# Performance work log

Hardware: AMD Instinct MI355X
Metric: run time of the kernel (lower is better)

## Reference

```python
import jax, jax.numpy as jnp
import numpy as np

H = 2048          # hidden_size
NH = 32           # num_attention_heads
NKV = 8           # num_key_value_heads
HD = H // NH      # head_dim = 64
GROUPS = NH // NKV
B, S = 1, 4096


def setup_inputs() -> dict:
    key = jax.random.key(0)
    k1, k2, k3, k4, k5 = jax.random.split(key, 5)
    hidden_states = jax.random.normal(k1, (B, S, H), dtype=jnp.float32)
    # additive causal mask [B, 1, S, S]
    causal = jnp.tril(jnp.ones((S, S), dtype=bool))
    attention_mask = jnp.where(causal, 0.0, jnp.finfo(jnp.float32).min)[None, None].astype(jnp.float32)
    scale = 0.02
    Wq = jax.random.normal(k2, (H, H), dtype=jnp.float32) * scale
    Wk = jax.random.normal(k3, (NKV * HD, H), dtype=jnp.float32) * scale
    Wv = jax.random.normal(k4, (NKV * HD, H), dtype=jnp.float32) * scale
    Wo = jax.random.normal(k5, (H, H), dtype=jnp.float32) * scale
    return {"hidden_states": hidden_states, "attention_mask": attention_mask,
            "Wq": Wq, "Wk": Wk, "Wv": Wv, "Wo": Wo}


def reference(hidden_states, attention_mask, Wq, Wk, Wv, Wo):
    bsz, q_len, _ = hidden_states.shape
    # projections (nn.Linear: x @ W.T)
    q = (hidden_states @ Wq.T).reshape(bsz, q_len, NH, HD).transpose(0, 2, 1, 3)   # [B,NH,S,HD]
    k = (hidden_states @ Wk.T).reshape(bsz, q_len, NKV, HD).transpose(0, 2, 1, 3)  # [B,NKV,S,HD]
    v = (hidden_states @ Wv.T).reshape(bsz, q_len, NKV, HD).transpose(0, 2, 1, 3)
    # repeat_kv: expand each KV head GROUPS times
    k = jnp.repeat(k, GROUPS, axis=1)  # [B,NH,S,HD]
    v = jnp.repeat(v, GROUPS, axis=1)
    attn_weights = jnp.einsum('bhqd,bhkd->bhqk', q, k) / jnp.sqrt(jnp.float32(HD))
    attn_weights = attn_weights + attention_mask
    attn_weights = jax.nn.softmax(attn_weights.astype(jnp.float32), axis=-1).astype(q.dtype)
    attn_output = jnp.einsum('bhqk,bhkd->bhqd', attn_weights, v)
    attn_output = attn_output.transpose(0, 2, 1, 3).reshape(bsz, q_len, H)
    return attn_output @ Wo.T
```

## Files before the change

kernel.cpp:

```cpp
#include <hip/hip_runtime.h>
#include <stdint.h>

#define S_LEN  4096
#define HDIM   2048
#define NHEADS 32
#define NKVH   8
#define HDSZ   64
#define KVDIM  (NKVH * HDSZ)
#define QKN    (HDIM + KVDIM)

typedef __bf16 v8bf16 __attribute__((ext_vector_type(8)));
typedef short  v4s    __attribute__((ext_vector_type(4)));
typedef float  v4f32  __attribute__((ext_vector_type(4)));

__device__ __forceinline__ unsigned short f2bf(float f) {
    uint32_t u = __builtin_bit_cast(uint32_t, f);
    uint32_t r = (u + 0x7fffu + ((u >> 16) & 1u)) >> 16;
    return (unsigned short)r;
}

__device__ __forceinline__ uint32_t pack_bf16(float a, float b) {
#if __has_builtin(__builtin_amdgcn_cvt_pk_bf16_f32)
    auto r = __builtin_amdgcn_cvt_pk_bf16_f32(a, b);
    return __builtin_bit_cast(uint32_t, r);
#else
    uint32_t ua = __builtin_bit_cast(uint32_t, a) + 0x8000u;
    uint32_t ub = __builtin_bit_cast(uint32_t, b) + 0x8000u;
    return (ua >> 16) | (ub & 0xffff0000u);
#endif
}

__device__ __forceinline__ float fast_exp2(float x) {
#if __has_builtin(__builtin_amdgcn_exp2f)
    return __builtin_amdgcn_exp2f(x);
#else
    float r; asm("v_exp_f32 %0, %1" : "=v"(r) : "v"(x)); return r;
#endif
}

__device__ __forceinline__ void async_load16(const void* g, void* l) {
    __builtin_amdgcn_global_load_lds((const __attribute__((address_space(1))) void*)g,
                                     (__attribute__((address_space(3))) void*)l,
                                     16, 0, 0);
}

#define SEG0 2097152
#define SEG1 3145728
#define SEG2 3407872
#define SEG3 3670016
#define SEGT 4718592
__global__ void cvt_all(const float* __restrict__ x,  const float* __restrict__ wq,
                        const float* __restrict__ wk, const float* __restrict__ wv,
                        const float* __restrict__ wo,
                        ushort4* __restrict__ xb, ushort4* __restrict__ wqkb,
                        ushort4* __restrict__ wvb, ushort4* __restrict__ wob,
                        float qscale)
{
    int i = blockIdx.x * blockDim.x + threadIdx.x;
    if (i >= SEGT) return;
    const float4* src; ushort4* dst; float s = 1.0f; int loc;
    if (i < SEG0)      { src = (const float4*)x;  dst = xb;   loc = i; }
    else if (i < SEG1) { src = (const float4*)wq; dst = wqkb; loc = i - SEG0; s = qscale; }
    else if (i < SEG2) { src = (const float4*)wk; dst = wqkb + 1048576; loc = i - SEG1; }
    else if (i < SEG3) { src = (const float4*)wv; dst = wvb;  loc = i - SEG2; }
    else               { src = (const float4*)wo; dst = wob;  loc = i - SEG3; }
    float4 f = src[loc];
    uint2 o;
    o.x = pack_bf16(f.x * s, f.y * s);
    o.y = pack_bf16(f.z * s, f.w * s);
    dst[loc] = __builtin_bit_cast(ushort4, o);
}


#define STAGE_A(buf, kh, t)                                                       \
    do {                                                                          \
        async_load16(A + aBase + (size_t)(t) * 64 + (kh) * 32,                    \
                     &smem[(buf) * 16384 + (kh) * 8192 + ldsSt]);                 \
        async_load16(A + aBase + (size_t)128 * Kd + (size_t)(t) * 64 + (kh) * 32, \
                     &smem[(buf) * 16384 + (kh) * 8192 + ldsSt + 4096]);          \
    } while (0)
#define STAGE_B(buf, kh, t)                                                       \
    do {                                                                          \
        async_load16(Bp + bBase + (size_t)(t) * 64 + (kh) * 32,                   \
                     &smem[32768 + (buf) * 16384 + (kh) * 8192 + ldsSt]);         \
        async_load16(Bp + bBase + (size_t)128 * Kd + (size_t)(t) * 64 + (kh) * 32,\
                     &smem[32768 + (buf) * 16384 + (kh) * 8192 + ldsSt + 4096]);  \
    } while (0)

#define LOAD_AF(khoff)                                                            \
    do {                                                                          \
        _Pragma("unroll")                                                         \
        for (int mi = 0; mi < 8; ++mi)                                            \
            af[mi] = *(const v8bf16*)&smem[curA + (khoff) + aRd + mi * 512];      \
    } while (0)

#define MFMA_PAIR(khoff, NI)                                                      \
    do {                                                                          \
        v8bf16 _b0 = *(const v8bf16*)&smem[curB + (khoff) + bRd + (NI) * 512];    \
        v8bf16 _b1 = *(const v8bf16*)&smem[curB + (khoff) + bRd + (NI) * 512 + 512];\
        __builtin_amdgcn_s_setprio(1);                                            \
        _Pragma("unroll")                                                         \
        for (int mi = 0; mi < 8; ++mi) {                                          \
            acc[mi][(NI)]     = __builtin_amdgcn_mfma_f32_16x16x32_bf16(af[mi], _b0, acc[mi][(NI)], 0, 0, 0);     \
            acc[mi][(NI) + 1] = __builtin_amdgcn_mfma_f32_16x16x32_bf16(af[mi], _b1, acc[mi][(NI) + 1], 0, 0, 0); \
        }                                                                         \
        __builtin_amdgcn_s_setprio(0);                                            \
    } while (0)

#define FENCE_BAR()                                                               \
    do {                                                                          \
        __builtin_amdgcn_sched_barrier(0);                                        \
        __builtin_amdgcn_s_barrier();                                             \
        __builtin_amdgcn_sched_barrier(0);                                        \
    } while (0)

#define WAITV(N) asm volatile("s_waitcnt vmcnt(" #N ")" ::: "memory")

template<bool F32OUT>
__device__ __forceinline__ void gemm256_body(
    const unsigned short* __restrict__ A,
    const unsigned short* __restrict__ Bp,
    void* __restrict__ Cout, int Nn, int Kd, int m0, int n0,
    unsigned short* __restrict__ smem)
{
    const int tid  = threadIdx.x;
    const int wave = tid >> 6;
    const int lane = tid & 63;
    const int lrow = lane & 15;
    const int quad = lane >> 4;
    const int wm = (wave >> 2) * 128;
    const int wn = (wave & 3) * 64;

    const int lr   = lane >> 2;
    const int sg4  = (lane & 3) ^ ((lane >> 3) & 3);
    const size_t aBase = (size_t)(m0 + wave * 16 + lr) * Kd + sg4 * 8;
    const size_t bBase = (size_t)(n0 + wave * 16 + lr) * Kd + sg4 * 8;
    const int ldsSt = wave * 512;

    const int rg4 = (quad ^ ((lrow >> 1) & 3)) * 8;
    const int aRd = (wm + lrow) * 32 + rg4;
    const int bRd = (wn + lrow) * 32 + rg4;

    const int NT = Kd >> 6;

    v4f32 acc[8][4];
#pragma unroll
    for (int mi = 0; mi < 8; ++mi)
#pragma unroll
        for (int ni = 0; ni < 4; ++ni)
#pragma unroll
            for (int r = 0; r < 4; ++r) acc[mi][ni][r] = 0.0f;

    STAGE_A(0, 0, 0); STAGE_B(0, 0, 0);
    STAGE_A(0, 1, 0); STAGE_B(0, 1, 0);
    STAGE_A(1, 0, 1); STAGE_B(1, 0, 1);
    WAITV(8);
    __builtin_amdgcn_s_barrier();
    __builtin_amdgcn_sched_barrier(0);

    v8bf16 af[8];
    for (int t = 0; t < NT - 2; ++t) {
        const int cur  = t & 1;
        const int nxt  = cur ^ 1;
        const int curA = cur * 16384;
        const int curB = 32768 + cur * 16384;

        STAGE_A(nxt, 1, t + 1);
        LOAD_AF(0);
        MFMA_PAIR(0, 0);
        FENCE_BAR();

        STAGE_B(nxt, 1, t + 1);
        MFMA_PAIR(0, 2);
        WAITV(8);
        FENCE_BAR();

        STAGE_A(cur, 0, t + 2);
        LOAD_AF(8192);
        MFMA_PAIR(8192, 0);
        FENCE_BAR();

        STAGE_B(cur, 0, t + 2);
        MFMA_PAIR(8192, 2);
        WAITV(8);
        FENCE_BAR();
    }

    {
        const int t = NT - 2;
        const int cur  = t & 1;
        const int nxt  = cur ^ 1;
        const int curA = cur * 16384;
        const int curB = 32768 + cur * 16384;

        STAGE_A(nxt, 1, t + 1);
        LOAD_AF(0);
        MFMA_PAIR(0, 0);
        FENCE_BAR();

        STAGE_B(nxt, 1, t + 1);
        MFMA_PAIR(0, 2);
        WAITV(8);
        FENCE_BAR();

        LOAD_AF(8192);
        MFMA_PAIR(8192, 0);
        FENCE_BAR();

        MFMA_PAIR(8192, 2);
        WAITV(4);
        FENCE_BAR();
    }

    {
        const int cur  = (NT - 1) & 1;
        const int curA = cur * 16384;
        const int curB = 32768 + cur * 16384;

        LOAD_AF(0);
        MFMA_PAIR(0, 0);
        FENCE_BAR();

        MFMA_PAIR(0, 2);
        WAITV(0);
        FENCE_BAR();

        LOAD_AF(8192);
        MFMA_PAIR(8192, 0);
        FENCE_BAR();

        MFMA_PAIR(8192, 2);
    }

    if (F32OUT) {
        float* Cf = (float*)Cout;
#pragma unroll
        for (int mi = 0; mi < 8; ++mi)
#pragma unroll
            for (int ni = 0; ni < 4; ++ni)
#pragma unroll
                for (int r = 0; r < 4; ++r) {
                    const int row = m0 + wm + mi * 16 + quad * 4 + r;
                    const int col = n0 + wn + ni * 16 + lrow;
                    Cf[(size_t)row * Nn + col] = acc[mi][ni][r];
                }
    } else {
        unsigned short* Cb = (unsigned short*)Cout;
#pragma unroll
        for (int mi = 0; mi < 8; ++mi)
#pragma unroll
            for (int ni = 0; ni < 4; ++ni)
#pragma unroll
                for (int r = 0; r < 4; ++r) {
                    const int row = m0 + wm + mi * 16 + quad * 4 + r;
                    const int col = n0 + wn + ni * 16 + lrow;
                    Cb[(size_t)row * Nn + col] = f2bf(acc[mi][ni][r]);
                }
    }
}

__global__ __launch_bounds__(512, 2)
void gemm_qkv256(const unsigned short* __restrict__ xb,
                 const unsigned short* __restrict__ Wqkb,
                 const unsigned short* __restrict__ Wvb,
                 unsigned short* __restrict__ QKb,
                 unsigned short* __restrict__ Vtb)
{
    __shared__ __align__(16) unsigned short smem[65536];
    const int bid = blockIdx.x;
    if (bid < 32) {
        gemm256_body<false>(Wvb, xb, Vtb, S_LEN, HDIM,
                            (bid >> 4) * 256, (bid & 15) * 256, smem);
    } else {
        const int b = bid - 32;
        gemm256_body<false>(xb, Wqkb, QKb, QKN, HDIM,
                            (b & 15) * 256, (b >> 4) * 256, smem);
    }
}

__global__ __launch_bounds__(512, 2)
void gemm_o256(const unsigned short* __restrict__ A,
               const unsigned short* __restrict__ B,
               float* __restrict__ Cout)
{
    __shared__ __align__(16) unsigned short smem[65536];
    const int bid = blockIdx.x;
    gemm256_body<true>(A, B, Cout, HDIM, HDIM,
                       (bid & 15) * 256, (bid >> 4) * 256, smem);
}

__global__ __launch_bounds__(256, 4)
void flash_attn(const unsigned short* __restrict__ QK,
                const unsigned short* __restrict__ Vt,
                unsigned short* __restrict__ O)
{
    __shared__ unsigned short smem[16384];
    unsigned short* Qs = smem;
    unsigned short* Ks = smem + 128 * 64;
    unsigned short* Vs = smem + 128 * 64 + 64 * 64;

    const int tid  = threadIdx.x;
    const int wave = tid >> 6;
    const int lane = tid & 63;
    const int lrow = lane & 15;
    const int quad = lane >> 4;

    const int h   = blockIdx.x;
    const int kvh = h >> 2;
    const int q0  = (gridDim.y - 1 - blockIdx.y) * 128;

    const int srow8 = lane >> 3;
    const int sgrp  = (lane & 7) ^ srow8;
    const v8bf16 v_one8 = __builtin_bit_cast(v8bf16,
        (uint4){0x3F803F80u, 0x3F803F80u, 0x3F803F80u, 0x3F803F80u});

    {
        const size_t gq = (size_t)(q0 + wave * 32 + srow8) * QKN + h * HDSZ + sgrp * 8;
#pragma unroll
        for (int i = 0; i < 4; ++i)
            async_load16(QK + gq + (size_t)(i * 8) * QKN, &Qs[(wave * 32 + i * 8) * 64]);
    }

    int kperm[2];
#pragma unroll
    for (int i = 0; i < 2; ++i) {
        const int slot = wave * 16 + i * 8 + srow8;
        const int nj = slot >> 4, sm = slot & 15;
        kperm[i] = 32 * (nj >> 1) + 8 * (sm >> 2) + 4 * (nj & 1) + (sm & 3);
    }

    v4f32 o_acc[2][4], l_acc[2];
#pragma unroll
    for (int mi = 0; mi < 2; ++mi) {
#pragma unroll
        for (int r = 0; r < 4; ++r) l_acc[mi][r] = 0.0f;
#pragma unroll
        for (int dj = 0; dj < 4; ++dj)
#pragma unroll
            for (int r = 0; r < 4; ++r) o_acc[mi][dj][r] = 0.0f;
    }

    const int rbase = q0 + wave * 32;
    const int njt   = (q0 >> 6) + 2;

    for (int j = 0; j < njt; ++j) {
        const int k0 = j * 64;
        __syncthreads();
        {
#pragma unroll
            for (int i = 0; i < 2; ++i) {
                const size_t gk = (size_t)(k0 + kperm[i]) * QKN
                                  + HDIM + kvh * HDSZ + sgrp * 8;
                async_load16(QK + gk, &Ks[(wave * 16 + i * 8) * 64]);
            }
            const size_t gv = (size_t)(kvh * HDSZ + wave * 16 + srow8) * S_LEN
                              + k0 + sgrp * 8;
            async_load16(Vt + gv,             &Vs[(wave * 16) * 64]);
            async_load16(Vt + gv + 8 * S_LEN, &Vs[(wave * 16 + 8) * 64]);
        }
        __syncthreads();

        if (k0 > rbase + 31) continue;

        v4f32 st[2][4];
#pragma unroll
        for (int mi = 0; mi < 2; ++mi)
#pragma unroll
            for (int nj = 0; nj < 4; ++nj)
#pragma unroll
                for (int r = 0; r < 4; ++r) st[mi][nj][r] = 0.0f;
#pragma unroll
        for (int kk = 0; kk < 2; ++kk) {
            const int swz = ((kk * 4 + quad) ^ (lrow & 7)) * 8;
            v8bf16 qa[2];
            qa[0] = *(const v8bf16*)&Qs[(wave * 32 + lrow) * 64 + swz];
            qa[1] = *(const v8bf16*)&Qs[(wave * 32 + 16 + lrow) * 64 + swz];
#pragma unroll
            for (int nj = 0; nj < 4; ++nj) {
                const v8bf16 kb = *(const v8bf16*)&Ks[(nj * 16 + lrow) * 64 + swz];
                st[0][nj] = __builtin_amdgcn_mfma_f32_16x16x32_bf16(kb, qa[0], st[0][nj], 0, 0, 0);
                st[1][nj] = __builtin_amdgcn_mfma_f32_16x16x32_bf16(kb, qa[1], st[1][nj], 0, 0, 0);
            }
        }

        if (k0 + 63 > rbase) {
#pragma unroll
            for (int mi = 0; mi < 2; ++mi) {
                const int qi = rbase + mi * 16 + lrow;
#pragma unroll
                for (int nj = 0; nj < 4; ++nj) {
                    const int kib = k0 + 32 * (nj >> 1) + 8 * quad + 4 * (nj & 1);
#pragma unroll
                    for (int r = 0; r < 4; ++r)
                        if (kib + r > qi) st[mi][nj][r] = -1e30f;
                }
            }
        }

        v8bf16 pk8[2][2];
#pragma unroll
        for (int mi = 0; mi < 2; ++mi) {
            uint2 pu[4];
#pragma unroll
            for (int nj = 0; nj < 4; ++nj) {
                const float p0 = fast_exp2(st[mi][nj][0]);
                const float p1 = fast_exp2(st[mi][nj][1]);
                const float p2 = fast_exp2(st[mi][nj][2]);
                const float p3 = fast_exp2(st[mi][nj][3]);
                pu[nj].x = pack_bf16(p0, p1);
                pu[nj].y = pack_bf16(p2, p3);
            }
            pk8[mi][0] = __builtin_bit_cast(v8bf16, (uint4){pu[0].x, pu[0].y, pu[1].x, pu[1].y});
            pk8[mi][1] = __builtin_bit_cast(v8bf16, (uint4){pu[2].x, pu[2].y, pu[3].x, pu[3].y});
        }

#pragma unroll
        for (int t = 0; t < 2; ++t) {
            const int swzv = ((t * 4 + quad) ^ (lrow & 7)) * 8;
            v8bf16 va[4];
#pragma unroll
            for (int dj = 0; dj < 4; ++dj)
                va[dj] = *(const v8bf16*)&Vs[(dj * 16 + lrow) * 64 + swzv];
#pragma unroll
            for (int dj = 0; dj < 4; ++dj) {
                o_acc[0][dj] = __builtin_amdgcn_mfma_f32_16x16x32_bf16(va[dj], pk8[0][t], o_acc[0][dj], 0, 0, 0);
                o_acc[1][dj] = __builtin_amdgcn_mfma_f32_16x16x32_bf16(va[dj], pk8[1][t], o_acc[1][dj], 0, 0, 0);
            }
            l_acc[0] = __builtin_amdgcn_mfma_f32_16x16x32_bf16(v_one8, pk8[0][t], l_acc[0], 0, 0, 0);
            l_acc[1] = __builtin_amdgcn_mfma_f32_16x16x32_bf16(v_one8, pk8[1][t], l_acc[1], 0, 0, 0);
        }
    }

    __syncthreads();
    unsigned short* Os = smem;
#pragma unroll
    for (int mi = 0; mi < 2; ++mi) {
        const float inv = 1.0f / l_acc[mi][0];
#pragma unroll
        for (int dj = 0; dj < 4; ++dj)
#pragma unroll
            for (int r = 0; r < 4; ++r)
                Os[(wave * 32 + mi * 16 + lrow) * 72 + dj * 16 + quad * 4 + r] =
                    f2bf(o_acc[mi][dj][r] * inv);
    }
    __syncthreads();
#pragma unroll
    for (int i = 0; i < 4; ++i) {
        const int idx = i * 256 + tid;
        const int row = idx >> 3, c8 = idx & 7;
        const uint4 vv = *(const uint4*)&Os[row * 72 + c8 * 8];
        *(uint4*)&O[(size_t)(q0 + row) * HDIM + h * HDSZ + c8 * 8] = vv;
    }
}

extern "C" void kernel_launch(void* const* d_in, const int* in_sizes, int n_in,
                              void* d_out, int out_size, void* d_ws, size_t ws_size,
                              hipStream_t stream)
{
    const float* x  = (const float*)d_in[0];
    const float* Wq = (const float*)d_in[2];
    const float* Wk = (const float*)d_in[3];
    const float* Wv = (const float*)d_in[4];
    const float* Wo = (const float*)d_in[5];
    float* out = (float*)d_out;

    unsigned short* xb   = (unsigned short*)d_ws;
    unsigned short* Wqkb = xb   + (size_t)S_LEN * HDIM;
    unsigned short* Wvb  = Wqkb + (size_t)QKN * HDIM;
    unsigned short* Wob  = Wvb  + (size_t)KVDIM * HDIM;
    unsigned short* QKb  = Wob  + (size_t)HDIM * HDIM;
    unsigned short* Vtb  = QKb  + (size_t)S_LEN * QKN;
    unsigned short* AOb  = xb;

    cvt_all<<<(SEGT + 255) / 256, 256, 0, stream>>>(
        x, Wq, Wk, Wv, Wo,
        (ushort4*)xb, (ushort4*)Wqkb, (ushort4*)Wvb, (ushort4*)Wob,
        0.18033688011f);

    gemm_qkv256<<<192, 512, 0, stream>>>(xb, Wqkb, Wvb, QKb, Vtb);

    flash_attn<<<dim3(NHEADS, S_LEN / 128), 256, 0, stream>>>(QKb, Vtb, AOb);

    gemm_o256<<<128, 512, 0, stream>>>(AOb, Wob, out);
}
```

Baseline: 343.5 us.

## Double-buffer K/V tiles in flash attention with async prefetch and MFMA priority

Splits the K/V shared-memory staging into two buffers so the next tile's async global-to-LDS loads are issued before computing on the current tile, waiting only on the older loads. Wraps MFMA blocks in s_setprio so compute waves get scheduling priority. Shared memory grows by half and the occupancy hint drops from 4 to 3 blocks per CU, trading occupancy for latency hiding.

```diff
diff --git a/kernel.cpp b/kernel.cpp
--- a/kernel.cpp
+++ b/kernel.cpp
@@ -289,15 +289,13 @@
                        (bid & 15) * 256, (bid >> 4) * 256, smem);
 }
 
-__global__ __launch_bounds__(256, 4)
+__global__ __launch_bounds__(256, 3)
 void flash_attn(const unsigned short* __restrict__ QK,
                 const unsigned short* __restrict__ Vt,
                 unsigned short* __restrict__ O)
 {
-    __shared__ unsigned short smem[16384];
+    __shared__ unsigned short smem[24576];
     unsigned short* Qs = smem;
-    unsigned short* Ks = smem + 128 * 64;
-    unsigned short* Vs = smem + 128 * 64 + 64 * 64;
 
     const int tid  = threadIdx.x;
     const int wave = tid >> 6;
@@ -329,6 +327,21 @@
         kperm[i] = 32 * (nj >> 1) + 8 * (sm >> 2) + 4 * (nj & 1) + (sm & 3);
     }
 
+    auto stage_kv = [&](int j) {
+        const int k0b = j * 64;
+        const int buf = (j & 1) * 4096;
+#pragma unroll
+        for (int i = 0; i < 2; ++i) {
+            const size_t gk = (size_t)(k0b + kperm[i]) * QKN
+                              + HDIM + kvh * HDSZ + sgrp * 8;
+            async_load16(QK + gk, &smem[8192 + buf + (wave * 16 + i * 8) * 64]);
+        }
+        const size_t gv = (size_t)(kvh * HDSZ + wave * 16 + srow8) * S_LEN
+                          + k0b + sgrp * 8;
+        async_load16(Vt + gv,             &smem[16384 + buf + (wave * 16) * 64]);
+        async_load16(Vt + gv + 8 * S_LEN, &smem[16384 + buf + (wave * 16 + 8) * 64]);
+    };
+
     v4f32 o_acc[2][4], l_acc[2];
 #pragma unroll
     for (int mi = 0; mi < 2; ++mi) {
@@ -343,92 +356,98 @@
     const int rbase = q0 + wave * 32;
     const int njt   = (q0 >> 6) + 2;
 
+    stage_kv(0);
+
     for (int j = 0; j < njt; ++j) {
-        const int k0 = j * 64;
-        __syncthreads();
-        {
-#pragma unroll
-            for (int i = 0; i < 2; ++i) {
-                const size_t gk = (size_t)(k0 + kperm[i]) * QKN
-                                  + HDIM + kvh * HDSZ + sgrp * 8;
-                async_load16(QK + gk, &Ks[(wave * 16 + i * 8) * 64]);
+        const int k0  = j * 64;
+        const int buf = (j & 1) * 4096;
+
+        if (j + 1 < njt) { stage_kv(j + 1); WAITV(4); }
+        else             { WAITV(0); }
+        __builtin_amdgcn_sched_barrier(0);
+        __builtin_amdgcn_s_barrier();
+        __builtin_amdgcn_sched_barrier(0);
+
+        if (k0 <= rbase + 31) {
+            const unsigned short* Ks = &smem[8192 + buf];
+            const unsigned short* Vs = &smem[16384 + buf];
+
+            v4f32 st[2][4];
+#pragma unroll
+            for (int mi = 0; mi < 2; ++mi)
+#pragma unroll
+                for (int nj = 0; nj < 4; ++nj)
+#pragma unroll
+                    for (int r = 0; r < 4; ++r) st[mi][nj][r] = 0.0f;
+#pragma unroll
+            for (int kk = 0; kk < 2; ++kk) {
+                const int swz = ((kk * 4 + quad) ^ (lrow & 7)) * 8;
+                v8bf16 qa[2];
+                qa[0] = *(const v8bf16*)&Qs[(wave * 32 + lrow) * 64 + swz];
+                qa[1] = *(const v8bf16*)&Qs[(wave * 32 + 16 + lrow) * 64 + swz];
+                __builtin_amdgcn_s_setprio(1);
+#pragma unroll
+                for (int nj = 0; nj < 4; ++nj) {
+                    const v8bf16 kb = *(const v8bf16*)&Ks[(nj * 16 + lrow) * 64 + swz];
+                    st[0][nj] = __builtin_amdgcn_mfma_f32_16x16x32_bf16(kb, qa[0], st[0][nj], 0, 0, 0);
+                    st[1][nj] = __builtin_amdgcn_mfma_f32_16x16x32_bf16(kb, qa[1], st[1][nj], 0, 0, 0);
+                }
+                __builtin_amdgcn_s_setprio(0);
             }
-            const size_t gv = (size_t)(kvh * HDSZ + wave * 16 + srow8) * S_LEN
-                              + k0 + sgrp * 8;
-            async_load16(Vt + gv,             &Vs[(wave * 16) * 64]);
-            async_load16(Vt + gv + 8 * S_LEN, &Vs[(wave * 16 + 8) * 64]);
-        }
-        __syncthreads();
-
-        if (k0 > rbase + 31) continue;
-
-        v4f32 st[2][4];
-#pragma unroll
-        for (int mi = 0; mi < 2; ++mi)
-#pragma unroll
-            for (int nj = 0; nj < 4; ++nj)
-#pragma unroll
-                for (int r = 0; r < 4; ++r) st[mi][nj][r] = 0.0f;
-#pragma unroll
-        for (int kk = 0; kk < 2; ++kk) {
-            const int swz = ((kk * 4 + quad) ^ (lrow & 7)) * 8;
-            v8bf16 qa[2];
-            qa[0] = *(const v8bf16*)&Qs[(wave * 32 + lrow) * 64 + swz];
-            qa[1] = *(const v8bf16*)&Qs[(wave * 32 + 16 + lrow) * 64 + swz];
-#pragma unroll
-            for (int nj = 0; nj < 4; ++nj) {
-                const v8bf16 kb = *(const v8bf16*)&Ks[(nj * 16 + lrow) * 64 + swz];
-                st[0][nj] = __builtin_amdgcn_mfma_f32_16x16x32_bf16(kb, qa[0], st[0][nj], 0, 0, 0);
-                st[1][nj] = __builtin_amdgcn_mfma_f32_16x16x32_bf16(kb, qa[1], st[1][nj], 0, 0, 0);
+
+            if (k0 + 63 > rbase) {
+#pragma unroll
+                for (int mi = 0; mi < 2; ++mi) {
+                    const int qi = rbase + mi * 16 + lrow;
+#pragma unroll
+                    for (int nj = 0; nj < 4; ++nj) {
+                        const int kib = k0 + 32 * (nj >> 1) + 8 * quad + 4 * (nj & 1);
+#pragma unroll
+                        for (int r = 0; r < 4; ++r)
+                            if (kib + r > qi) st[mi][nj][r] = -1e30f;
+                    }
+                }
+            }
+
+            v8bf16 pk8[2][2];
+#pragma unroll
+            for (int mi = 0; mi < 2; ++mi) {
+                uint2 pu[4];
+#pragma unroll
+                for (int nj = 0; nj < 4; ++nj) {
+                    const float p0 = fast_exp2(st[mi][nj][0]);
+                    const float p1 = fast_exp2(st[mi][nj][1]);
+                    const float p2 = fast_exp2(st[mi][nj][2]);
+                    const float p3 = fast_exp2(st[mi][nj][3]);
+                    pu[nj].x = pack_bf16(p0, p1);
+                    pu[nj].y = pack_bf16(p2, p3);
+                }
+                pk8[mi][0] = __builtin_bit_cast(v8bf16, (uint4){pu[0].x, pu[0].y, pu[1].x, pu[1].y});
+                pk8[mi][1] = __builtin_bit_cast(v8bf16, (uint4){pu[2].x, pu[2].y, pu[3].x, pu[3].y});
+            }
+
+#pragma unroll
+            for (int t = 0; t < 2; ++t) {
+                const int swzv = ((t * 4 + quad) ^ (lrow & 7)) * 8;
+                v8bf16 va[4];
+#pragma unroll
+                for (int dj = 0; dj < 4; ++dj)
+                    va[dj] = *(const v8bf16*)&Vs[(dj * 16 + lrow) * 64 + swzv];
+                __builtin_amdgcn_s_setprio(1);
+#pragma unroll
+                for (int dj = 0; dj < 4; ++dj) {
+                    o_acc[0][dj] = __builtin_amdgcn_mfma_f32_16x16x32_bf16(va[dj], pk8[0][t], o_acc[0][dj], 0, 0, 0);
+                    o_acc[1][dj] = __builtin_amdgcn_mfma_f32_16x16x32_bf16(va[dj], pk8[1][t], o_acc[1][dj], 0, 0, 0);
+                }
+                l_acc[0] = __builtin_amdgcn_mfma_f32_16x16x32_bf16(v_one8, pk8[0][t], l_acc[0], 0, 0, 0);
+                l_acc[1] = __builtin_amdgcn_mfma_f32_16x16x32_bf16(v_one8, pk8[1][t], l_acc[1], 0, 0, 0);
+                __builtin_amdgcn_s_setprio(0);
             }
         }
 
-        if (k0 + 63 > rbase) {
-#pragma unroll
-            for (int mi = 0; mi < 2; ++mi) {
-                const int qi = rbase + mi * 16 + lrow;
-#pragma unroll
-                for (int nj = 0; nj < 4; ++nj) {
-                    const int kib = k0 + 32 * (nj >> 1) + 8 * quad + 4 * (nj & 1);
-#pragma unroll
-                    for (int r = 0; r < 4; ++r)
-                        if (kib + r > qi) st[mi][nj][r] = -1e30f;
-                }
-            }
-        }
-
-        v8bf16 pk8[2][2];
-#pragma unroll
-        for (int mi = 0; mi < 2; ++mi) {
-            uint2 pu[4];
-#pragma unroll
-            for (int nj = 0; nj < 4; ++nj) {
-                const float p0 = fast_exp2(st[mi][nj][0]);
-                const float p1 = fast_exp2(st[mi][nj][1]);
-                const float p2 = fast_exp2(st[mi][nj][2]);
-                const float p3 = fast_exp2(st[mi][nj][3]);
-                pu[nj].x = pack_bf16(p0, p1);
-                pu[nj].y = pack_bf16(p2, p3);
-            }
-            pk8[mi][0] = __builtin_bit_cast(v8bf16, (uint4){pu[0].x, pu[0].y, pu[1].x, pu[1].y});
-            pk8[mi][1] = __builtin_bit_cast(v8bf16, (uint4){pu[2].x, pu[2].y, pu[3].x, pu[3].y});
-        }
-
-#pragma unroll
-        for (int t = 0; t < 2; ++t) {
-            const int swzv = ((t * 4 + quad) ^ (lrow & 7)) * 8;
-            v8bf16 va[4];
-#pragma unroll
-            for (int dj = 0; dj < 4; ++dj)
-                va[dj] = *(const v8bf16*)&Vs[(dj * 16 + lrow) * 64 + swzv];
-#pragma unroll
-            for (int dj = 0; dj < 4; ++dj) {
-                o_acc[0][dj] = __builtin_amdgcn_mfma_f32_16x16x32_bf16(va[dj], pk8[0][t], o_acc[0][dj], 0, 0, 0);
-                o_acc[1][dj] = __builtin_amdgcn_mfma_f32_16x16x32_bf16(va[dj], pk8[1][t], o_acc[1][dj], 0, 0, 0);
-            }
-            l_acc[0] = __builtin_amdgcn_mfma_f32_16x16x32_bf16(v_one8, pk8[0][t], l_acc[0], 0, 0, 0);
-            l_acc[1] = __builtin_amdgcn_mfma_f32_16x16x32_bf16(v_one8, pk8[1][t], l_acc[1], 0, 0, 0);
-        }
+        __builtin_amdgcn_sched_barrier(0);
+        __builtin_amdgcn_s_barrier();
+        __builtin_amdgcn_sched_barrier(0);
     }
 
     __syncthreads();
```

Result: no change. 341.7 us (-0.5%).
